# Optimization experiments

Hardware: AMD Instinct MI355X
Metric: run time of the kernel (lower is better)

## Reference

```python
import jax, jax.numpy as jnp
import numpy as np
import math

N, T, D, H = 128, 512, 1024, 1024

def setup_inputs() -> dict:
    key = jax.random.key(0)
    k1, k2, k3, k4 = jax.random.split(key, 4)
    x = jax.random.normal(k1, (N, T, D), dtype=jnp.float32)
    h0 = jax.random.normal(k2, (N, H), dtype=jnp.float32)
    Wx = jax.random.normal(k3, (D, H), dtype=jnp.float32) / math.sqrt(D)
    Wh = jax.random.normal(k4, (H, H), dtype=jnp.float32) / math.sqrt(H)
    b = jnp.zeros((H,), dtype=jnp.float32)
    return {"x": x, "h0": h0, "Wx": Wx, "Wh": Wh, "b": b}

def reference(x, h0, Wx, Wh, b):
    # Precompute input-to-hidden projections for all timesteps at once (same math
    # as per-step x_t @ Wx, but a single large GEMM).
    xw = jnp.einsum('ntd,dh->nth', x, Wx) + b  # (N, T, H)

    def step(h_prev, xw_t):
        h_next = jnp.tanh(xw_t + h_prev @ Wh)
        return h_next, h_next

    # scan over time axis: move T to leading axis
    _, hs = jax.lax.scan(step, h0, jnp.swapaxes(xw, 0, 1))  # hs: (T, N, H)
    return jnp.swapaxes(hs, 0, 1)  # (N, T, H)
```

## Files before the change

### kernel.cpp

```cpp
#include <hip/hip_runtime.h>
#include <math.h>

#define N_ 128
#define T_ 512
#define D_ 1024
#define H_ 1024

__global__ __launch_bounds__(256) void gemm_xw(
    const float* __restrict__ A,
    const float* __restrict__ B,
    const float* __restrict__ bias,
    float* __restrict__ C)
{
    __shared__ float As[8][128];
    __shared__ float Bs[8][128];

    const int tid = threadIdx.x;
    const int m0 = blockIdx.x * 128;
    const int n0 = blockIdx.y * 128;

    const int la_m = tid & 127;
    const int la_k = (tid >> 7) * 4;
    const int lb_k = tid >> 5;
    const int lb_n = (tid & 31) * 4;

    const int tx = tid & 15;
    const int ty = tid >> 4;
    const int cm = ty * 8;
    const int cn = tx * 8;

    float acc[8][8];
#pragma unroll
    for (int i = 0; i < 8; i++)
#pragma unroll
        for (int j = 0; j < 8; j++) acc[i][j] = 0.f;

    const float* aptr = A + (long)(m0 + la_m) * D_ + la_k;
    const float* bptr = B + (long)lb_k * H_ + n0 + lb_n;

    for (int k0 = 0; k0 < D_; k0 += 8) {
        float4 av = *(const float4*)(aptr + k0);
        float4 bv = *(const float4*)(bptr + (long)k0 * H_);
        As[la_k + 0][la_m] = av.x;
        As[la_k + 1][la_m] = av.y;
        As[la_k + 2][la_m] = av.z;
        As[la_k + 3][la_m] = av.w;
        *(float4*)&Bs[lb_k][lb_n] = bv;
        __syncthreads();
#pragma unroll
        for (int k = 0; k < 8; k++) {
            float a0[8], b0[8];
            *(float4*)&a0[0] = *(const float4*)&As[k][cm];
            *(float4*)&a0[4] = *(const float4*)&As[k][cm + 4];
            *(float4*)&b0[0] = *(const float4*)&Bs[k][cn];
            *(float4*)&b0[4] = *(const float4*)&Bs[k][cn + 4];
#pragma unroll
            for (int i = 0; i < 8; i++)
#pragma unroll
                for (int j = 0; j < 8; j++)
                    acc[i][j] = fmaf(a0[i], b0[j], acc[i][j]);
        }
        __syncthreads();
    }

#pragma unroll
    for (int i = 0; i < 8; i++) {
        long row = (long)(m0 + cm + i) * H_ + n0;
#pragma unroll
        for (int j = 0; j < 8; j += 4) {
            float4 v;
            v.x = acc[i][j + 0] + bias[n0 + cn + j + 0];
            v.y = acc[i][j + 1] + bias[n0 + cn + j + 1];
            v.z = acc[i][j + 2] + bias[n0 + cn + j + 2];
            v.w = acc[i][j + 3] + bias[n0 + cn + j + 3];
            *(float4*)&C[row + cn + j] = v;
        }
    }
}

__global__ __launch_bounds__(256) void rnn_step(
    const float* __restrict__ hprev, long hstride,
    const float* __restrict__ Wh,
    float* __restrict__ out_t)
{
    __shared__ float hs[H_];
    const int n = blockIdx.x >> 2;
    const int j = ((blockIdx.x & 3) << 8) + threadIdx.x;

    *(float4*)&hs[threadIdx.x * 4] =
        *(const float4*)&hprev[(long)n * hstride + threadIdx.x * 4];
    __syncthreads();

    const float* wcol = Wh + j;
    float acc0 = 0.f, acc1 = 0.f, acc2 = 0.f, acc3 = 0.f;
#pragma unroll 4
    for (int k = 0; k < H_; k += 4) {
        acc0 = fmaf(hs[k + 0], wcol[(long)(k + 0) * H_], acc0);
        acc1 = fmaf(hs[k + 1], wcol[(long)(k + 1) * H_], acc1);
        acc2 = fmaf(hs[k + 2], wcol[(long)(k + 2) * H_], acc2);
        acc3 = fmaf(hs[k + 3], wcol[(long)(k + 3) * H_], acc3);
    }
    long oidx = (long)n * (T_ * H_) + j;
    out_t[oidx] = tanhf(out_t[oidx] + (acc0 + acc1) + (acc2 + acc3));
}

extern "C" void kernel_launch(void* const* d_in, const int* in_sizes, int n_in,
                              void* d_out, int out_size, void* d_ws, size_t ws_size,
                              hipStream_t stream) {
    const float* x  = (const float*)d_in[0];
    const float* h0 = (const float*)d_in[1];
    const float* Wx = (const float*)d_in[2];
    const float* Wh = (const float*)d_in[3];
    const float* b  = (const float*)d_in[4];
    float* out = (float*)d_out;

    dim3 g1((N_ * T_) / 128, H_ / 128);
    gemm_xw<<<g1, 256, 0, stream>>>(x, Wx, b, out);

    for (int t = 0; t < T_; t++) {
        const float* hp = (t == 0) ? h0 : (out + (long)(t - 1) * H_);
        long hstride = (t == 0) ? (long)H_ : (long)T_ * H_;
        rnn_step<<<dim3(N_ * 4), 256, 0, stream>>>(hp, hstride, Wh,
                                                   out + (long)t * H_);
    }
}
```

Before: 13.70 ms.

## Tile recurrent step over batch rows and columns to reuse Wh loads

Rewrites the per-step recurrent GEMM kernel so each block handles 16 batch rows by 32 hidden columns. Each thread computes four columns for one row over half of K, and the two halves are combined through shared memory. Every Wh element loaded is now reused across 16 batch rows instead of one, which cuts global/L2 traffic for Wh on each step. In exchange the grid shrinks to 256 blocks, each holding about 66KB of shared memory, which may lower occupancy.

```diff
diff --git a/kernel.cpp b/kernel.cpp
--- a/kernel.cpp
+++ b/kernel.cpp
@@ -83,25 +83,59 @@
     const float* __restrict__ Wh,
     float* __restrict__ out_t)
 {
-    __shared__ float hs[H_];
-    const int n = blockIdx.x >> 2;
-    const int j = ((blockIdx.x & 3) << 8) + threadIdx.x;
+    __shared__ float hs[16][1028];
+    __shared__ float red[16][33];
 
-    *(float4*)&hs[threadIdx.x * 4] =
-        *(const float4*)&hprev[(long)n * hstride + threadIdx.x * 4];
+    const int tid = threadIdx.x;
+    const int m0 = (blockIdx.x >> 5) * 16;
+    const int n0 = (blockIdx.x & 31) * 32;
+
+    {
+        const int lr = tid >> 4;
+        const int lc = (tid & 15) * 4;
+        const float* src = hprev + (long)(m0 + lr) * hstride;
+#pragma unroll
+        for (int i = 0; i < 16; i++) {
+            *(float4*)&hs[lr][lc + i * 64] = *(const float4*)&src[lc + i * 64];
+        }
+    }
     __syncthreads();
 
-    const float* wcol = Wh + j;
-    float acc0 = 0.f, acc1 = 0.f, acc2 = 0.f, acc3 = 0.f;
-#pragma unroll 4
-    for (int k = 0; k < H_; k += 4) {
-        acc0 = fmaf(hs[k + 0], wcol[(long)(k + 0) * H_], acc0);
-        acc1 = fmaf(hs[k + 1], wcol[(long)(k + 1) * H_], acc1);
-        acc2 = fmaf(hs[k + 2], wcol[(long)(k + 2) * H_], acc2);
-        acc3 = fmaf(hs[k + 3], wcol[(long)(k + 3) * H_], acc3);
+    const int ks = tid >> 7;
+    const int r  = (tid >> 3) & 15;
+    const int cg = tid & 7;
+
+    const float* wp   = Wh + (long)(ks * 512) * H_ + n0 + cg * 4;
+    const float* hrow = &hs[r][ks * 512];
+
+    float4 acc = make_float4(0.f, 0.f, 0.f, 0.f);
+#pragma unroll 8
+    for (int k = 0; k < 512; k++) {
+        float hv = hrow[k];
+        float4 w = *(const float4*)(wp + (long)k * H_);
+        acc.x = fmaf(hv, w.x, acc.x);
+        acc.y = fmaf(hv, w.y, acc.y);
+        acc.z = fmaf(hv, w.z, acc.z);
+        acc.w = fmaf(hv, w.w, acc.w);
     }
-    long oidx = (long)n * (T_ * H_) + j;
-    out_t[oidx] = tanhf(out_t[oidx] + (acc0 + acc1) + (acc2 + acc3));
+
+    if (ks == 1) {
+        red[r][cg * 4 + 0] = acc.x;
+        red[r][cg * 4 + 1] = acc.y;
+        red[r][cg * 4 + 2] = acc.z;
+        red[r][cg * 4 + 3] = acc.w;
+    }
+    __syncthreads();
+    if (ks == 0) {
+        long o = (long)(m0 + r) * (T_ * H_) + n0 + cg * 4;
+        float4 xw4 = *(const float4*)&out_t[o];
+        float4 res;
+        res.x = tanhf(xw4.x + acc.x + red[r][cg * 4 + 0]);
+        res.y = tanhf(xw4.y + acc.y + red[r][cg * 4 + 1]);
+        res.z = tanhf(xw4.z + acc.z + red[r][cg * 4 + 2]);
+        res.w = tanhf(xw4.w + acc.w + red[r][cg * 4 + 3]);
+        *(float4*)&out_t[o] = res;
+    }
 }
 
 extern "C" void kernel_launch(void* const* d_in, const int* in_sizes, int n_in,
@@ -120,7 +154,7 @@
     for (int t = 0; t < T_; t++) {
         const float* hp = (t == 0) ? h0 : (out + (long)(t - 1) * H_);
         long hstride = (t == 0) ? (long)H_ : (long)T_ * H_;
-        rnn_step<<<dim3(N_ * 4), 256, 0, stream>>>(hp, hstride, Wh,
-                                                   out + (long)t * H_);
+        rnn_step<<<dim3(256), 256, 0, stream>>>(hp, hstride, Wh,
+                                                out + (long)t * H_);
     }
 }
```

After: 11.52 ms. -15.9%, faster.
